# Performance work log

Measured on AMD Instinct MI355X. Metric: run time of the kernel, lower is better.

The kernel has to match this reference:

```python
import jax, jax.numpy as jnp
import numpy as np
from jax import lax

# Mamba2-130m-like config (quantized wrapper)
D_MODEL = 768
N_LAYER = 8
D_STATE = 128
D_CONV = 4
EXPAND = 2
HEADDIM = 64
VOCAB = 50288
D_INNER = EXPAND * D_MODEL            # 1536
NHEADS = D_INNER // HEADDIM           # 24
D_IN_PROJ = 2 * D_INNER + 2 * D_STATE + NHEADS  # 3352 (ngroups=1)
CONV_DIM = D_INNER + 2 * D_STATE      # 1792
EPS = 1e-5
BATCH, SEQLEN = 1, 1024

# QuantRMSNorm rsqrt lookup table (256 entries over [1e-5, 10])
LUT_X = jnp.linspace(1e-5, 10.0, 256)
LUT_Y = 1.0 / jnp.sqrt(LUT_X)


def _fake_quant_linear(w):
    # QuantLinear: torch.quantize_per_tensor(scale=0.1, zero_point=0, qint8).dequantize()
    return jnp.clip(jnp.round(w / 0.1), -128, 127) * 0.1


def setup_inputs():
    key = jax.random.key(0)
    ks = jax.random.split(key, 12)
    input_ids = jax.random.randint(ks[0], (BATCH, SEQLEN), 0, VOCAB)
    embedding = jax.random.normal(ks[1], (VOCAB, D_MODEL), jnp.float32)
    norm_w = jnp.ones((N_LAYER, D_MODEL), jnp.float32)
    in_proj_w = _fake_quant_linear(
        jax.random.normal(ks[2], (N_LAYER, D_IN_PROJ, D_MODEL), jnp.float32) * (D_MODEL ** -0.5))
    # QuantConv1d: asymmetric per-tensor int8 weight; forward uses q_weight.float()
    # WITHOUT subtracting zero_point (as in the source), times (w_scale * x_scale).
    conv_f = jax.random.normal(ks[3], (N_LAYER, CONV_DIM, D_CONV), jnp.float32) * (D_CONV ** -0.5)
    wmin = conv_f.min(axis=(1, 2), keepdims=True)
    wmax = conv_f.max(axis=(1, 2), keepdims=True)
    conv_scale = (wmax - wmin) / (255.0 + 1e-8)   # qmax - qmin = 255
    zp = jnp.round(-wmin / conv_scale)
    q_conv_w = jnp.clip(jnp.round(conv_f / conv_scale) + zp, -128, 127)
    conv_scale = conv_scale.reshape(N_LAYER)
    conv_b = jax.random.normal(ks[4], (N_LAYER, CONV_DIM), jnp.float32) * 0.02
    dt = jax.random.uniform(ks[5], (N_LAYER, NHEADS), jnp.float32, 0.001, 0.1)
    dt_bias = jnp.log(jnp.expm1(dt))              # inverse softplus
    A_log = jnp.log(jax.random.uniform(ks[6], (N_LAYER, NHEADS), jnp.float32, 1.0, 16.0))
    D_param = jnp.ones((N_LAYER, NHEADS), jnp.float32)
    mixer_norm_w = jnp.ones((N_LAYER, D_INNER), jnp.float32)
    out_proj_w = _fake_quant_linear(
        jax.random.normal(ks[7], (N_LAYER, D_MODEL, D_INNER), jnp.float32) * (D_INNER ** -0.5))
    normf_w = jnp.ones((D_MODEL,), jnp.float32)
    lm_head_w = _fake_quant_linear(
        jax.random.normal(ks[8], (VOCAB, D_MODEL), jnp.float32) * (D_MODEL ** -0.5))
    return dict(input_ids=input_ids, embedding=embedding, norm_w=norm_w, in_proj_w=in_proj_w,
                q_conv_w=q_conv_w, conv_scale=conv_scale, conv_b=conv_b, dt_bias=dt_bias,
                A_log=A_log, D_param=D_param, mixer_norm_w=mixer_norm_w, out_proj_w=out_proj_w,
                normf_w=normf_w, lm_head_w=lm_head_w)


def _lut_rmsnorm(x, w):
    # QuantRMSNorm: rsqrt approximated by a 256-entry LUT via bucketize
    rms = jnp.mean(x * x, axis=-1, keepdims=True) + EPS       # [b,l,1]
    idx = jnp.clip(jnp.searchsorted(LUT_X, rms), 0, 255)      # torch.bucketize (right=False)
    return x * LUT_Y[idx] * w


def _quant_act(x):
    # quantize_activation: symmetric per-tensor int8
    s = jnp.max(jnp.abs(x)) / (127.0 + 1e-8)
    return jnp.clip(jnp.round(x / s), -128, 127), s


def _mixer(u, in_w, qcw, cscale, cb, dtb, a_log, d_p, mnw, out_w):
    b, l, _ = u.shape
    zxbcdt = jnp.einsum('bld,ed->ble', u, in_w)               # QuantLinear (pre-fake-quantized w)
    z = zxbcdt[..., :D_INNER]
    xBC = zxbcdt[..., D_INNER:D_INNER + CONV_DIM]
    dt = jax.nn.softplus(zxbcdt[..., -NHEADS:] + dtb)         # [b,l,h]
    # QuantConv1d: depthwise causal conv on int8-quantized activation
    xq, xs = _quant_act(xBC)
    xp = jnp.pad(xq, ((0, 0), (D_CONV - 1, 0), (0, 0)))
    conv = sum(xp[:, k:k + l, :] * qcw[:, k] for k in range(D_CONV)) + cb
    xBC = jax.nn.silu(conv * (cscale * xs))
    x = xBC[..., :D_INNER].reshape(b, l, NHEADS, HEADDIM)
    Bm = xBC[..., D_INNER:D_INNER + D_STATE]                  # ngroups=1, shared over heads
    Cm = xBC[..., D_INNER + D_STATE:]
    dA = dt * (-jnp.exp(a_log))                               # [b,l,h]
    xdt = x * dt[..., None]
    def step(hs, inp):
        xdt_t, dA_t, B_t, C_t = inp
        hs = jnp.exp(dA_t)[..., None, None] * hs + xdt_t[..., None] * B_t[:, None, None, :]
        return hs, jnp.einsum('bhpn,bn->bhp', hs, C_t)
    h0 = jnp.zeros((b, NHEADS, HEADDIM, D_STATE), u.dtype)
    _, ys = lax.scan(step, h0, (xdt.swapaxes(0, 1), dA.swapaxes(0, 1),
                                Bm.swapaxes(0, 1), Cm.swapaxes(0, 1)))
    y = ys.swapaxes(0, 1) + x * d_p[None, None, :, None]      # [b,l,h,p]
    y = y.reshape(b, l, D_INNER)
    y = y * jax.nn.silu(z)                                    # gated RMSNorm (float, not LUT)
    y = y * lax.rsqrt(jnp.mean(y * y, axis=-1, keepdims=True) + EPS) * mnw
    return jnp.einsum('ble,de->bld', y, out_w)                # QuantLinear out_proj


def reference(input_ids, embedding, norm_w, in_proj_w, q_conv_w, conv_scale, conv_b,
              dt_bias, A_log, D_param, mixer_norm_w, out_proj_w, normf_w, lm_head_w):
    x = embedding[input_ids]
    for i in range(N_LAYER):
        y = _mixer(_lut_rmsnorm(x, norm_w[i]), in_proj_w[i], q_conv_w[i], conv_scale[i],
                   conv_b[i], dt_bias[i], A_log[i], D_param[i], mixer_norm_w[i], out_proj_w[i])
        x = y + x
    x = _lut_rmsnorm(x, normf_w)
    return jnp.einsum('bld,vd->blv', x, lm_head_w)            # logits [b,l,vocab]
```

## Files before the change

### kernel.cpp

```cpp
#include <hip/hip_runtime.h>
#include <math.h>

#define D_MODEL 768
#define N_LAYER 8
#define D_STATE 128
#define D_CONV 4
#define HEADDIM 64
#define D_INNER 1536
#define NHEADS 24
#define D_IN_PROJ 3352
#define CONV_DIM 1792
#define SEQLEN 1024
#define VOCAB 50288
#define EPS 1e-5f
#define T_SEG 32
#define NSEG  32

typedef __bf16 bf16x8 __attribute__((ext_vector_type(8)));
typedef float f32x4 __attribute__((ext_vector_type(4)));

__device__ inline unsigned short f2bf(float x) {
    union { float f; unsigned u; } v; v.f = x;
    unsigned r = v.u + 0x7fffu + ((v.u >> 16) & 1u);
    return (unsigned short)(r >> 16);
}
__device__ inline float bf2f(unsigned short b) {
    union { unsigned u; float f; } v; v.u = ((unsigned)b) << 16;
    return v.f;
}

__global__ void k_embed(const int* __restrict__ ids, const float* __restrict__ emb,
                        float* __restrict__ x) {
    int t = blockIdx.x;
    int id = ids[t];
    const float* er = emb + (long)id * D_MODEL;
    for (int d = threadIdx.x; d < D_MODEL; d += blockDim.x)
        x[(long)t * D_MODEL + d] = er[d];
}

__global__ void k_lutnorm(const float* __restrict__ x, const float* __restrict__ w,
                          float* __restrict__ out, unsigned short* __restrict__ oh,
                          unsigned short* __restrict__ ol, unsigned* __restrict__ mx) {
    __shared__ float sbuf[256];
    int t = blockIdx.x;
    if (t == 0 && threadIdx.x == 0) *mx = 0u;
    const float* xr = x + (long)t * D_MODEL;
    float ss = 0.f;
    for (int d = threadIdx.x; d < D_MODEL; d += 256) { float v = xr[d]; ss += v * v; }
    sbuf[threadIdx.x] = ss; __syncthreads();
    for (int s = 128; s > 0; s >>= 1) {
        if (threadIdx.x < s) sbuf[threadIdx.x] += sbuf[threadIdx.x + s];
        __syncthreads();
    }
    float rms = sbuf[0] / (float)D_MODEL + EPS;
    const float X0 = 1e-5f;
    const float STEP = (10.0f - 1e-5f) / 255.0f;
    int idx = (int)ceilf((rms - X0) / STEP);
    idx = min(max(idx, 0), 255);
    while (idx > 0 && (X0 + (float)(idx - 1) * STEP) >= rms) --idx;
    while (idx < 255 && (X0 + (float)idx * STEP) < rms) ++idx;
    float scale = 1.0f / sqrtf(X0 + (float)idx * STEP);
    for (int d = threadIdx.x; d < D_MODEL; d += 256) {
        float v = xr[d] * scale * w[d];
        out[(long)t * D_MODEL + d] = v;
        unsigned short h = f2bf(v);
        oh[(long)t * D_MODEL + d] = h;
        ol[(long)t * D_MODEL + d] = f2bf(v - bf2f(h));
    }
}

__global__ void k_f2bf(const float* __restrict__ src, unsigned short* __restrict__ dst, int n8) {
    int i = blockIdx.x * 256 + threadIdx.x;
    int stride = gridDim.x * 256;
    for (; i < n8; i += stride) {
        const float* s = src + (size_t)i * 8;
        float4 a = *(const float4*)s, b = *(const float4*)(s + 4);
        float ff[8] = {a.x, a.y, a.z, a.w, b.x, b.y, b.z, b.w};
        unsigned short h[8];
#pragma unroll
        for (int j = 0; j < 8; ++j) h[j] = f2bf(ff[j]);
        uint4 u = make_uint4(h[0] | (h[1] << 16), h[2] | (h[3] << 16),
                             h[4] | (h[5] << 16), h[6] | (h[7] << 16));
        *(uint4*)(dst + (size_t)i * 8) = u;
    }
}

__global__ void k_f2bf2(const float* __restrict__ src, unsigned short* __restrict__ dh,
                        unsigned short* __restrict__ dl, int n8) {
    int i = blockIdx.x * 256 + threadIdx.x;
    int stride = gridDim.x * 256;
    for (; i < n8; i += stride) {
        const float* s = src + (size_t)i * 8;
        float4 a = *(const float4*)s, b = *(const float4*)(s + 4);
        float ff[8] = {a.x, a.y, a.z, a.w, b.x, b.y, b.z, b.w};
        unsigned short h[8], lo[8];
#pragma unroll
        for (int j = 0; j < 8; ++j) {
            h[j] = f2bf(ff[j]);
            lo[j] = f2bf(ff[j] - bf2f(h[j]));
        }
        uint4 uh = make_uint4(h[0] | (h[1] << 16), h[2] | (h[3] << 16),
                              h[4] | (h[5] << 16), h[6] | (h[7] << 16));
        uint4 ul = make_uint4(lo[0] | (lo[1] << 16), lo[2] | (lo[3] << 16),
                              lo[4] | (lo[5] << 16), lo[6] | (lo[7] << 16));
        *(uint4*)(dh + (size_t)i * 8) = uh;
        *(uint4*)(dl + (size_t)i * 8) = ul;
    }
}

template <int PASSES, bool AMAX>
__global__ __launch_bounds__(512) void k_gemm_big(
    const unsigned short* __restrict__ Agh, const unsigned short* __restrict__ Agl,
    const unsigned short* __restrict__ Bgh, const unsigned short* __restrict__ Bgl,
    float* __restrict__ C, int N, int NT, int K, unsigned* __restrict__ mx) {
    const int i = blockIdx.x;
    const int rxcd = i & 7, xm = (i >> 3) & 7, q = i >> 6;
    const int y = q * 8 + rxcd;
    if (y >= NT) return;
    const int bm = xm * 128, bn = y * 128;

    constexpr int SMEM_BYTES = (PASSES == 3) ? 32768 : 16896;
    __shared__ __align__(16) char smem[SMEM_BYTES];
    unsigned short (*Ah)[128][8] = (unsigned short(*)[128][8])(smem);
    unsigned short (*Bh)[128][8] = (unsigned short(*)[128][8])(smem + 8192);
    unsigned short (*Al)[128][8] = (unsigned short(*)[128][8])(smem + 16384);
    unsigned short (*Bl)[128][8] = (unsigned short(*)[128][8])(smem + 24576);

    const int tid = threadIdx.x;
    const int r = tid >> 2, g = tid & 3;
    const int rsw = r ^ (g << 1);
    const int w = tid >> 6, l = tid & 63;
    const int wm = w >> 2, wn = w & 3;
    const int lr = l & 15, lg = l >> 4;

    f32x4 acc[4][2];
#pragma unroll
    for (int m = 0; m < 4; ++m)
#pragma unroll
        for (int n = 0; n < 2; ++n) acc[m][n] = (f32x4){0.f, 0.f, 0.f, 0.f};

    for (int k0 = 0; k0 < K; k0 += 32) {
        {
            *(uint4*)&Ah[g][rsw][0] = *(const uint4*)(Agh + (size_t)(bm + r) * K + k0 + g * 8);
            if constexpr (PASSES == 3)
                *(uint4*)&Al[g][rsw][0] = *(const uint4*)(Agl + (size_t)(bm + r) * K + k0 + g * 8);
            int rB = bn + r;
            uint4 zb = make_uint4(0, 0, 0, 0);
            uint4 ubh = (rB < N) ? *(const uint4*)(Bgh + (size_t)rB * K + k0 + g * 8) : zb;
            *(uint4*)&Bh[g][rsw][0] = ubh;
            if constexpr (PASSES == 3) {
                uint4 ubl = (rB < N) ? *(const uint4*)(Bgl + (size_t)rB * K + k0 + g * 8) : zb;
                *(uint4*)&Bl[g][rsw][0] = ubl;
            }
        }
        __syncthreads();

        bf16x8 ah[4], al_[4], bh[2], bl_[2];
#pragma unroll
        for (int m = 0; m < 4; ++m) {
            int row = (wm * 64 + m * 16 + lr) ^ (lg << 1);
            ah[m] = *(const bf16x8*)&Ah[lg][row][0];
            if constexpr (PASSES == 3) al_[m] = *(const bf16x8*)&Al[lg][row][0];
        }
#pragma unroll
        for (int n = 0; n < 2; ++n) {
            int row = (wn * 32 + n * 16 + lr) ^ (lg << 1);
            bh[n] = *(const bf16x8*)&Bh[lg][row][0];
            if constexpr (PASSES == 3) bl_[n] = *(const bf16x8*)&Bl[lg][row][0];
        }
#pragma unroll
        for (int m = 0; m < 4; ++m)
#pragma unroll
            for (int n = 0; n < 2; ++n) {
                acc[m][n] = __builtin_amdgcn_mfma_f32_16x16x32_bf16(ah[m], bh[n], acc[m][n], 0, 0, 0);
                if constexpr (PASSES == 3) {
                    acc[m][n] = __builtin_amdgcn_mfma_f32_16x16x32_bf16(al_[m], bh[n], acc[m][n], 0, 0, 0);
                    acc[m][n] = __builtin_amdgcn_mfma_f32_16x16x32_bf16(ah[m], bl_[n], acc[m][n], 0, 0, 0);
                }
            }
        __syncthreads();
    }

    if (AMAX) {
        float lmax = 0.f;
#pragma unroll
        for (int m = 0; m < 4; ++m)
#pragma unroll
            for (int n = 0; n < 2; ++n) {
                int col = bn + wn * 32 + n * 16 + lr;
                if (col >= D_INNER && col < D_INNER + CONV_DIM) {
#pragma unroll
                    for (int r4 = 0; r4 < 4; ++r4)
                        lmax = fmaxf(lmax, fabsf(acc[m][n][r4]));
                }
            }
#pragma unroll
        for (int s = 1; s <= 32; s <<= 1) lmax = fmaxf(lmax, __shfl_xor(lmax, s));
        if (l == 0) atomicMax(mx, __float_as_uint(lmax));
    }

    float (*cbuf)[132] = (float(*)[132])smem;
    const int clrow = tid >> 4;
    const int clcol = (tid & 15) * 8;
#pragma unroll
    for (int c = 0; c < 4; ++c) {
        if (c) __syncthreads();
        if (wm == (c >> 1)) {
#pragma unroll
            for (int mm = 0; mm < 2; ++mm) {
                int m = (c & 1) * 2 + mm;
                int lrow = mm * 16 + lg * 4;
#pragma unroll
                for (int n = 0; n < 2; ++n) {
                    int lcol = wn * 32 + n * 16 + lr;
#pragma unroll
                    for (int r4 = 0; r4 < 4; ++r4) cbuf[lrow + r4][lcol] = acc[m][n][r4];
                }
            }
        }
        __syncthreads();
        int grow = bm + c * 32 + clrow;
        int gcol = bn + clcol;
        float4 v0 = *(const float4*)&cbuf[clrow][clcol];
        float4 v1 = *(const float4*)&cbuf[clrow][clcol + 4];
        float* dst = C + (size_t)grow * N + gcol;
        if (gcol + 8 <= N) {
            *(float4*)dst = v0;
            *(float4*)(dst + 4) = v1;
        } else if (gcol < N) {
            float tmp[8] = {v0.x, v0.y, v0.z, v0.w, v1.x, v1.y, v1.z, v1.w};
            for (int j = 0; j < 8; ++j)
                if (gcol + j < N) dst[j] = tmp[j];
        }
    }
}

__global__ __launch_bounds__(256) void k_gemm_out(
    const unsigned short* __restrict__ Agh, const unsigned short* __restrict__ Agl,
    const unsigned short* __restrict__ Bgh, const unsigned short* __restrict__ Bgl,
    float* __restrict__ C) {
    const int K = 1536, N = 768;
    const int i = blockIdx.x;
    const int rxcd = i & 7, xm = (i >> 3) & 15, q = i >> 7;
    const int y = q * 8 + rxcd;
    if (y >= 12) return;
    const int bm = xm * 64, bn = y * 64;

    __shared__ __align__(16) char smem[16384];
    unsigned short (*Ah)[64][8] = (unsigned short(*)[64][8])(smem);
    unsigned short (*Bh)[64][8] = (unsigned short(*)[64][8])(smem + 4096);
    unsigned short (*Al)[64][8] = (unsigned short(*)[64][8])(smem + 8192);
    unsigned short (*Bl)[64][8] = (unsigned short(*)[64][8])(smem + 12288);

    const int tid = threadIdx.x;
    const int r = tid >> 2, g = tid & 3;
    const int rsw = r ^ (g << 1);
    const int w = tid >> 6, l = tid & 63;
    const int wm = w >> 1, wn = w & 1;
    const int lr = l & 15, lg = l >> 4;

    f32x4 acc[2][2];
#pragma unroll
    for (int m = 0; m < 2; ++m)
#pragma unroll
        for (int n = 0; n < 2; ++n) acc[m][n] = (f32x4){0.f, 0.f, 0.f, 0.f};

    for (int k0 = 0; k0 < K; k0 += 32) {
        *(uint4*)&Ah[g][rsw][0] = *(const uint4*)(Agh + (size_t)(bm + r) * K + k0 + g * 8);
        *(uint4*)&Al[g][rsw][0] = *(const uint4*)(Agl + (size_t)(bm + r) * K + k0 + g * 8);
        *(uint4*)&Bh[g][rsw][0] = *(const uint4*)(Bgh + (size_t)(bn + r) * K + k0 + g * 8);
        *(uint4*)&Bl[g][rsw][0] = *(const uint4*)(Bgl + (size_t)(bn + r) * K + k0 + g * 8);
        __syncthreads();

        bf16x8 ah[2], al_[2], bh[2], bl_[2];
#pragma unroll
        for (int m = 0; m < 2; ++m) {
            int row = (wm * 32 + m * 16 + lr) ^ (lg << 1);
            ah[m] = *(const bf16x8*)&Ah[lg][row][0];
            al_[m] = *(const bf16x8*)&Al[lg][row][0];
        }
#pragma unroll
        for (int n = 0; n < 2; ++n) {
            int row = (wn * 32 + n * 16 + lr) ^ (lg << 1);
            bh[n] = *(const bf16x8*)&Bh[lg][row][0];
            bl_[n] = *(const bf16x8*)&Bl[lg][row][0];
        }
#pragma unroll
        for (int m = 0; m < 2; ++m)
#pragma unroll
            for (int n = 0; n < 2; ++n) {
                acc[m][n] = __builtin_amdgcn_mfma_f32_16x16x32_bf16(ah[m], bh[n], acc[m][n], 0, 0, 0);
                acc[m][n] = __builtin_amdgcn_mfma_f32_16x16x32_bf16(al_[m], bh[n], acc[m][n], 0, 0, 0);
                acc[m][n] = __builtin_amdgcn_mfma_f32_16x16x32_bf16(ah[m], bl_[n], acc[m][n], 0, 0, 0);
            }
        __syncthreads();
    }

    float (*cbuf)[68] = (float(*)[68])smem;
    const int clrow = tid >> 3;
    const int clcol = (tid & 7) * 8;
#pragma unroll
    for (int c = 0; c < 2; ++c) {
        if (c) __syncthreads();
        if (wm == c) {
#pragma unroll
            for (int m = 0; m < 2; ++m) {
                int lrow = m * 16 + lg * 4;
#pragma unroll
                for (int n = 0; n < 2; ++n) {
                    int lcol = wn * 32 + n * 16 + lr;
#pragma unroll
                    for (int r4 = 0; r4 < 4; ++r4) cbuf[lrow + r4][lcol] = acc[m][n][r4];
                }
            }
        }
        __syncthreads();
        int grow = bm + c * 32 + clrow;
        float* dst = C + (size_t)grow * N + bn + clcol;
        float4 v0 = *(const float4*)&cbuf[clrow][clcol];
        float4 v1 = *(const float4*)&cbuf[clrow][clcol + 4];
        float4 r0 = *(const float4*)dst;
        float4 r1 = *(const float4*)(dst + 4);
        r0.x += v0.x; r0.y += v0.y; r0.z += v0.z; r0.w += v0.w;
        r1.x += v1.x; r1.y += v1.y; r1.z += v1.z; r1.w += v1.w;
        *(float4*)dst = r0;
        *(float4*)(dst + 4) = r1;
    }
}

template <int PASSES, bool ACCUM>
__global__ __launch_bounds__(256) void k_gemm_mfma(const float* __restrict__ A,
                                                   const float* __restrict__ B,
                                                   float* __restrict__ C,
                                                   int M, int N, int K) {
    __shared__ __align__(16) unsigned short Ah[4][128][8];
    __shared__ __align__(16) unsigned short Bh[4][128][8];
    __shared__ __align__(16) unsigned short Al[(PASSES == 3) ? 4 : 1][128][8];
    __shared__ __align__(16) unsigned short Bl[(PASSES == 3) ? 4 : 1][128][8];
    const int bm = blockIdx.x * 128, bn = blockIdx.y * 128;
    const int tid = threadIdx.x;
    const int rr = tid >> 2, g = tid & 3;
    const int w = tid >> 6, l = tid & 63;
    const int wm = w >> 1, wn = w & 1;
    const int lr = l & 15, lg = l >> 4;
    f32x4 acc[4][4];
#pragma unroll
    for (int m = 0; m < 4; ++m)
#pragma unroll
        for (int n = 0; n < 4; ++n) acc[m][n] = (f32x4){0.f, 0.f, 0.f, 0.f};
    for (int k0 = 0; k0 < K; k0 += 32) {
#pragma unroll
        for (int half = 0; half < 2; ++half) {
            int r = rr + half * 64;
            {
                const float* s = A + (size_t)(bm + r) * K + k0 + g * 8;
                float4 f0 = *(const float4*)s;
                float4 f1 = *(const float4*)(s + 4);
                float ff[8] = {f0.x, f0.y, f0.z, f0.w, f1.x, f1.y, f1.z, f1.w};
                unsigned short h[8], lo[8];
#pragma unroll
                for (int ii = 0; ii < 8; ++ii) {
                    h[ii] = f2bf(ff[ii]);
                    if (PASSES == 3) lo[ii] = f2bf(ff[ii] - bf2f(h[ii]));
                }
                *(uint4*)&Ah[g][r][0] = make_uint4(h[0] | (h[1] << 16), h[2] | (h[3] << 16),
                                                   h[4] | (h[5] << 16), h[6] | (h[7] << 16));
                if (PASSES == 3)
                    *(uint4*)&Al[g][r][0] = make_uint4(lo[0] | (lo[1] << 16), lo[2] | (lo[3] << 16),
                                                       lo[4] | (lo[5] << 16), lo[6] | (lo[7] << 16));
            }
            {
                int rB = bn + r;
                float ff[8] = {0.f, 0.f, 0.f, 0.f, 0.f, 0.f, 0.f, 0.f};
                if (rB < N) {
                    const float* s = B + (size_t)rB * K + k0 + g * 8;
                    float4 f0 = *(const float4*)s;
                    float4 f1 = *(const float4*)(s + 4);
                    ff[0] = f0.x; ff[1] = f0.y; ff[2] = f0.z; ff[3] = f0.w;
                    ff[4] = f1.x; ff[5] = f1.y; ff[6] = f1.z; ff[7] = f1.w;
                }
                unsigned short h[8], lo[8];
#pragma unroll
                for (int ii = 0; ii < 8; ++ii) {
                    h[ii] = f2bf(ff[ii]);
                    if (PASSES == 3) lo[ii] = f2bf(ff[ii] - bf2f(h[ii]));
                }
                *(uint4*)&Bh[g][r][0] = make_uint4(h[0] | (h[1] << 16), h[2] | (h[3] << 16),
                                                   h[4] | (h[5] << 16), h[6] | (h[7] << 16));
                if (PASSES == 3)
                    *(uint4*)&Bl[g][r][0] = make_uint4(lo[0] | (lo[1] << 16), lo[2] | (lo[3] << 16),
                                                       lo[4] | (lo[5] << 16), lo[6] | (lo[7] << 16));
            }
        }
        __syncthreads();
        bf16x8 ah[4], bh[4], al_[4], bl_[4];
#pragma unroll
        for (int m = 0; m < 4; ++m) {
            int row = wm * 64 + m * 16 + lr;
            ah[m] = *(const bf16x8*)&Ah[lg][row][0];
            if (PASSES == 3) al_[m] = *(const bf16x8*)&Al[lg][row][0];
        }
#pragma unroll
        for (int n = 0; n < 4; ++n) {
            int row = wn * 64 + n * 16 + lr;
            bh[n] = *(const bf16x8*)&Bh[lg][row][0];
            if (PASSES == 3) bl_[n] = *(const bf16x8*)&Bl[lg][row][0];
        }
#pragma unroll
        for (int m = 0; m < 4; ++m)
#pragma unroll
            for (int n = 0; n < 4; ++n) {
                acc[m][n] = __builtin_amdgcn_mfma_f32_16x16x32_bf16(ah[m], bh[n], acc[m][n], 0, 0, 0);
                if (PASSES == 3) {
                    acc[m][n] = __builtin_amdgcn_mfma_f32_16x16x32_bf16(al_[m], bh[n], acc[m][n], 0, 0, 0);
                    acc[m][n] = __builtin_amdgcn_mfma_f32_16x16x32_bf16(ah[m], bl_[n], acc[m][n], 0, 0, 0);
                }
            }
        __syncthreads();
    }
#pragma unroll
    for (int m = 0; m < 4; ++m) {
        int row0 = bm + wm * 64 + m * 16 + lg * 4;
#pragma unroll
        for (int n = 0; n < 4; ++n) {
            int col = bn + wn * 64 + n * 16 + lr;
            if (col < N) {
#pragma unroll
                for (int r4 = 0; r4 < 4; ++r4) {
                    size_t off = (size_t)(row0 + r4) * N + col;
                    if (ACCUM) C[off] += acc[m][n][r4]; else C[off] = acc[m][n][r4];
                }
            }
        }
    }
}

__global__ void k_absmax(const float* __restrict__ zx, unsigned* __restrict__ out) {
    __shared__ float sbuf[256];
    float m = 0.f;
    int total = SEQLEN * CONV_DIM;
    for (int i = blockIdx.x * blockDim.x + threadIdx.x; i < total; i += gridDim.x * blockDim.x) {
        int t = i / CONV_DIM, c = i - t * CONV_DIM;
        float v = fabsf(zx[(long)t * D_IN_PROJ + D_INNER + c]);
        m = fmaxf(m, v);
    }
    sbuf[threadIdx.x] = m; __syncthreads();
    for (int s = 128; s > 0; s >>= 1) {
        if (threadIdx.x < s) sbuf[threadIdx.x] = fmaxf(sbuf[threadIdx.x], sbuf[threadIdx.x + s]);
        __syncthreads();
    }
    if (threadIdx.x == 0) atomicMax(out, __float_as_uint(sbuf[0]));
}

__global__ void k_convq(const float* __restrict__ zx, const float* __restrict__ qcw,
                        const float* __restrict__ cb, const float* __restrict__ cscale,
                        const unsigned* __restrict__ mx, float* __restrict__ xact) {
    int i = blockIdx.x * blockDim.x + threadIdx.x;
    if (i >= SEQLEN * CONV_DIM) return;
    float s = __uint_as_float(*mx) / (127.0f + 1e-8f);
    float inv_s = 1.0f / s;
    int t = i / CONV_DIM, c = i - t * CONV_DIM;
    float acc = cb[c];
#pragma unroll
    for (int k = 0; k < D_CONV; ++k) {
        int tt = t - (D_CONV - 1) + k;
        if (tt >= 0) {
            float q = rintf(zx[(size_t)tt * D_IN_PROJ + D_INNER + c] * inv_s);
            q = fminf(fmaxf(q, -128.0f), 127.0f);
            acc = fmaf(q, qcw[c * D_CONV + k], acc);
        }
    }
    float v = acc * (cscale[0] * s);
    xact[i] = v / (1.0f + expf(-v));
}

__global__ __launch_bounds__(256) void k_scan_local(
    const float* __restrict__ xact, const float* __restrict__ zx,
    const float* __restrict__ dtbias, const float* __restrict__ A_log,
    float* __restrict__ y, float* __restrict__ hloc, float* __restrict__ dpre) {
    const int head = blockIdx.x;
    const int seg  = blockIdx.y;
    const int tid  = threadIdx.x;
    const int p  = tid >> 2;
    const int nc = tid & 3;
    const int t0 = seg * T_SEG;

    __shared__ float4 sB4[T_SEG][32];
    __shared__ float4 sC4[T_SEG][32];
    __shared__ float  sX[T_SEG][64];
    __shared__ float  sDt[T_SEG], sA[T_SEG];

#pragma unroll
    for (int it = 0; it < 4; ++it) {
        int slot = tid + it * 256;
        int t = slot >> 5, c4 = slot & 31;
        const float* rowp = xact + (size_t)(t0 + t) * CONV_DIM + D_INNER;
        float4 bv = *(const float4*)(rowp + c4 * 4);
        float4 cv = *(const float4*)(rowp + D_STATE + c4 * 4);
        int grp = c4 >> 3, r4 = c4 & 7;
        int sl = grp * 8 + ((r4 + 2 * grp) & 7);
        sB4[t][sl] = bv;
        sC4[t][sl] = cv;
    }
#pragma unroll
    for (int it = 0; it < 2; ++it) {
        int slot = tid + it * 256;
        int t = slot >> 4, c4 = slot & 15;
        *(float4*)&sX[t][c4 * 4] =
            *(const float4*)(xact + (size_t)(t0 + t) * CONV_DIM + head * HEADDIM + c4 * 4);
    }
    if (tid < T_SEG) {
        float v = zx[(size_t)(t0 + tid) * D_IN_PROJ + (D_INNER + CONV_DIM) + head] + dtbias[head];
        float dtv = fmaxf(v, 0.f) + log1pf(expf(-fabsf(v)));
        sDt[tid] = dtv;
        sA[tid] = expf(dtv * (-expf(A_log[head])));
    }
    __syncthreads();

    float h[32];
#pragma unroll
    for (int j = 0; j < 32; ++j) h[j] = 0.f;
    float d = 1.f;
    float* yrow = y + head * HEADDIM + p;

    for (int t = 0; t < T_SEG; ++t) {
        float a = sA[t], dtv = sDt[t];
        float xdt = sX[t][p] * dtv;
        d *= a;
        float acc = 0.f;
#pragma unroll
        for (int j4 = 0; j4 < 8; ++j4) {
            int sl = nc * 8 + ((j4 + 2 * nc) & 7);
            float4 Bv = sB4[t][sl];
            float4 Cv = sC4[t][sl];
            h[j4 * 4 + 0] = fmaf(a, h[j4 * 4 + 0], xdt * Bv.x); acc = fmaf(h[j4 * 4 + 0], Cv.x, acc);
            h[j4 * 4 + 1] = fmaf(a, h[j4 * 4 + 1], xdt * Bv.y); acc = fmaf(h[j4 * 4 + 1], Cv.y, acc);
            h[j4 * 4 + 2] = fmaf(a, h[j4 * 4 + 2], xdt * Bv.z); acc = fmaf(h[j4 * 4 + 2], Cv.z, acc);
            h[j4 * 4 + 3] = fmaf(a, h[j4 * 4 + 3], xdt * Bv.w); acc = fmaf(h[j4 * 4 + 3], Cv.w, acc);
        }
        acc += __shfl_xor(acc, 1);
        acc += __shfl_xor(acc, 2);
        if (nc == 0) yrow[(size_t)(t0 + t) * D_INNER] = acc;
        if (tid == 0) dpre[(head * NSEG + seg) * T_SEG + t] = d;
    }

    float* hb = hloc + ((size_t)(head * NSEG + seg) * 64 + p) * 128 + nc * 32;
#pragma unroll
    for (int j4 = 0; j4 < 8; ++j4)
        *(float4*)(hb + j4 * 4) =
            make_float4(h[j4 * 4], h[j4 * 4 + 1], h[j4 * 4 + 2], h[j4 * 4 + 3]);
}

__global__ __launch_bounds__(256) void k_scan_seg(float* __restrict__ hloc,
                                                  const float* __restrict__ dpre) {
    int g = blockIdx.x * 256 + threadIdx.x;
    int head = g >> 11;
    int e4 = g & 2047;
    float4 run = make_float4(0.f, 0.f, 0.f, 0.f);
    for (int seg = 0; seg < NSEG; ++seg) {
        float d = dpre[(head * NSEG + seg) * T_SEG + (T_SEG - 1)];
        float4* ptr = (float4*)hloc + (size_t)(head * NSEG + seg) * 2048 + e4;
        float4 v = *ptr;
        run.x = fmaf(d, run.x, v.x);
        run.y = fmaf(d, run.y, v.y);
        run.z = fmaf(d, run.z, v.z);
        run.w = fmaf(d, run.w, v.w);
        *ptr = run;
    }
}

__global__ __launch_bounds__(256) void k_scan_fix(
    const float* __restrict__ xact, const float* __restrict__ hloc,
    const float* __restrict__ dpre, float* __restrict__ y) {
    const int head = blockIdx.x;
    const int seg  = blockIdx.y + 1;
    const int tid  = threadIdx.x;
    const int p  = tid >> 2;
    const int nc = tid & 3;
    const int t0 = seg * T_SEG;

    __shared__ float4 sC4[T_SEG][32];
    __shared__ float  sD[T_SEG];

#pragma unroll
    for (int it = 0; it < 4; ++it) {
        int slot = tid + it * 256;
        int t = slot >> 5, c4 = slot & 31;
        float4 cv = *(const float4*)(xact + (size_t)(t0 + t) * CONV_DIM + D_INNER + D_STATE + c4 * 4);
        int grp = c4 >> 3, r4 = c4 & 7;
        sC4[t][grp * 8 + ((r4 + 2 * grp) & 7)] = cv;
    }
    if (tid < T_SEG) sD[tid] = dpre[(head * NSEG + seg) * T_SEG + tid];
    __syncthreads();

    float H[32];
    const float* hb = hloc + ((size_t)(head * NSEG + seg - 1) * 64 + p) * 128 + nc * 32;
#pragma unroll
    for (int j4 = 0; j4 < 8; ++j4) {
        float4 v = *(const float4*)(hb + j4 * 4);
        H[j4 * 4 + 0] = v.x; H[j4 * 4 + 1] = v.y; H[j4 * 4 + 2] = v.z; H[j4 * 4 + 3] = v.w;
    }
    float* yrow = y + head * HEADDIM + p;
    for (int t = 0; t < T_SEG; ++t) {
        float acc = 0.f;
#pragma unroll
        for (int j4 = 0; j4 < 8; ++j4) {
            int sl = nc * 8 + ((j4 + 2 * nc) & 7);
            float4 Cv = sC4[t][sl];
            acc = fmaf(H[j4 * 4 + 0], Cv.x, acc);
            acc = fmaf(H[j4 * 4 + 1], Cv.y, acc);
            acc = fmaf(H[j4 * 4 + 2], Cv.z, acc);
            acc = fmaf(H[j4 * 4 + 3], Cv.w, acc);
        }
        acc += __shfl_xor(acc, 1);
        acc += __shfl_xor(acc, 2);
        if (nc == 0) yrow[(size_t)(t0 + t) * D_INNER] += sD[t] * acc;
    }
}

__global__ void k_gatenorm(const float* __restrict__ ybuf, const float* __restrict__ zx,
                           const float* __restrict__ xact, const float* __restrict__ dpar,
                           const float* __restrict__ mnw, float* __restrict__ y3,
                           unsigned short* __restrict__ y3h, unsigned short* __restrict__ y3l) {
    __shared__ float sbuf[256];
    int t = blockIdx.x;
    const float* yr = ybuf + (long)t * D_INNER;
    const float* zr = zx + (long)t * D_IN_PROJ;
    const float* xa = xact + (long)t * CONV_DIM;
    float vals[6];
    float ss = 0.f;
#pragma unroll
    for (int j = 0; j < 6; ++j) {
        int e = threadIdx.x + j * 256;
        float z = zr[e];
        float v = (yr[e] + xa[e] * dpar[e >> 6]) * (z / (1.0f + expf(-z)));
        vals[j] = v; ss += v * v;
    }
    sbuf[threadIdx.x] = ss; __syncthreads();
    for (int s = 128; s > 0; s >>= 1) {
        if (threadIdx.x < s) sbuf[threadIdx.x] += sbuf[threadIdx.x + s];
        __syncthreads();
    }
    float scale = 1.0f / sqrtf(sbuf[0] / (float)D_INNER + EPS);
#pragma unroll
    for (int j = 0; j < 6; ++j) {
        int e = threadIdx.x + j * 256;
        float v = vals[j] * scale * mnw[e];
        y3[(long)t * D_INNER + e] = v;
        unsigned short h = f2bf(v);
        y3h[(long)t * D_INNER + e] = h;
        y3l[(long)t * D_INNER + e] = f2bf(v - bf2f(h));
    }
}

extern "C" void kernel_launch(void* const* d_in, const int* in_sizes, int n_in,
                              void* d_out, int out_size, void* d_ws, size_t ws_size,
                              hipStream_t stream) {
    const int*   ids    = (const int*)d_in[0];
    const float* emb    = (const float*)d_in[1];
    const float* norm_w = (const float*)d_in[2];
    const float* inw    = (const float*)d_in[3];
    const float* qconv  = (const float*)d_in[4];
    const float* cscale = (const float*)d_in[5];
    const float* convb  = (const float*)d_in[6];
    const float* dtbias = (const float*)d_in[7];
    const float* alog   = (const float*)d_in[8];
    const float* dpar   = (const float*)d_in[9];
    const float* mnw    = (const float*)d_in[10];
    const float* outw   = (const float*)d_in[11];
    const float* normf  = (const float*)d_in[12];
    const float* lmw    = (const float*)d_in[13];
    float* out = (float*)d_out;

    char* base = (char*)d_ws;
    size_t off = 0;
    auto alloc = [&](size_t bytes) { char* r = base + off; off = (off + bytes + 255) & ~(size_t)255; return r; };

    float* xres = (float*)alloc((size_t)SEQLEN * D_MODEL * 4);
    float* u    = (float*)alloc((size_t)SEQLEN * D_MODEL * 4);
    float* zx   = (float*)alloc((size_t)SEQLEN * D_IN_PROJ * 4);
    float* xact = (float*)alloc((size_t)SEQLEN * CONV_DIM * 4);
    float* ybuf = (float*)alloc((size_t)SEQLEN * D_INNER * 4);
    float* y3   = (float*)alloc((size_t)SEQLEN * D_INNER * 4);
    float* hloc = (float*)alloc((size_t)NHEADS * NSEG * HEADDIM * D_STATE * 4);
    float* dpre = (float*)alloc((size_t)NHEADS * NSEG * T_SEG * 4);
    unsigned* mx = (unsigned*)alloc(64);
    unsigned short* uh  = (unsigned short*)alloc((size_t)SEQLEN * D_MODEL * 2);
    unsigned short* ul  = (unsigned short*)alloc((size_t)SEQLEN * D_MODEL * 2);
    unsigned short* y3h = (unsigned short*)alloc((size_t)SEQLEN * D_INNER * 2);
    unsigned short* y3l = (unsigned short*)alloc((size_t)SEQLEN * D_INNER * 2);
    unsigned short* lmwh = (unsigned short*)alloc((size_t)VOCAB * D_MODEL * 2);
    size_t core_need = off;
    unsigned short* inwh = (unsigned short*)alloc((size_t)N_LAYER * D_IN_PROJ * D_MODEL * 2);
    unsigned short* inwl = (unsigned short*)alloc((size_t)N_LAYER * D_IN_PROJ * D_MODEL * 2);
    unsigned short* outwh = (unsigned short*)alloc((size_t)N_LAYER * D_MODEL * D_INNER * 2);
    unsigned short* outwl = (unsigned short*)alloc((size_t)N_LAYER * D_MODEL * D_INNER * 2);
    size_t full_need = off;
    const bool big = (ws_size >= full_need);
    (void)core_need;

    k_embed<<<SEQLEN, 256, 0, stream>>>(ids, emb, xres);
    k_f2bf<<<2048, 256, 0, stream>>>(lmw, lmwh, (VOCAB * D_MODEL) / 8);
    if (big) {
        k_f2bf2<<<2048, 256, 0, stream>>>(inw, inwh, inwl, (N_LAYER * D_IN_PROJ * D_MODEL) / 8);
        k_f2bf2<<<2048, 256, 0, stream>>>(outw, outwh, outwl, (N_LAYER * D_MODEL * D_INNER) / 8);
    }

    int nq = SEQLEN * CONV_DIM;
    const int NT_IN = (D_IN_PROJ + 127) / 128;
    const int NT_LM = (VOCAB + 127) / 128;
    for (int l = 0; l < N_LAYER; ++l) {
        k_lutnorm<<<SEQLEN, 256, 0, stream>>>(xres, norm_w + l * D_MODEL, u, uh, ul, mx);
        if (big) {
            int nblk = 8 * 8 * ((NT_IN + 7) / 8);
            k_gemm_big<3, true><<<nblk, 512, 0, stream>>>(
                uh, ul, inwh + (size_t)l * D_IN_PROJ * D_MODEL,
                inwl + (size_t)l * D_IN_PROJ * D_MODEL, zx, D_IN_PROJ, NT_IN, D_MODEL, mx);
        } else {
            dim3 g1(SEQLEN / 128, NT_IN);
            k_gemm_mfma<3, false><<<g1, 256, 0, stream>>>(u, inw + (size_t)l * D_IN_PROJ * D_MODEL,
                                                          zx, SEQLEN, D_IN_PROJ, D_MODEL);
            k_absmax<<<256, 256, 0, stream>>>(zx, mx);
        }
        k_convq<<<(nq + 255) / 256, 256, 0, stream>>>(zx, qconv + l * CONV_DIM * D_CONV,
                                                      convb + l * CONV_DIM, cscale + l, mx, xact);
        dim3 gs1(NHEADS, NSEG);
        k_scan_local<<<gs1, 256, 0, stream>>>(xact, zx, dtbias + l * NHEADS, alog + l * NHEADS,
                                              ybuf, hloc, dpre);
        k_scan_seg<<<192, 256, 0, stream>>>(hloc, dpre);
        dim3 gs3(NHEADS, NSEG - 1);
        k_scan_fix<<<gs3, 256, 0, stream>>>(xact, hloc, dpre, ybuf);
        k_gatenorm<<<SEQLEN, 256, 0, stream>>>(ybuf, zx, xact, dpar + l * NHEADS,
                                               mnw + l * D_INNER, y3, y3h, y3l);
        if (big) {
            k_gemm_out<<<256, 256, 0, stream>>>(y3h, y3l,
                outwh + (size_t)l * D_MODEL * D_INNER, outwl + (size_t)l * D_MODEL * D_INNER, xres);
        } else {
            dim3 g2(SEQLEN / 128, (D_MODEL + 127) / 128);
            k_gemm_mfma<3, true><<<g2, 256, 0, stream>>>(y3, outw + (size_t)l * D_MODEL * D_INNER,
                                                         xres, SEQLEN, D_MODEL, D_INNER);
        }
    }
    k_lutnorm<<<SEQLEN, 256, 0, stream>>>(xres, normf, u, uh, ul, mx);
    {
        int nblk = 8 * 8 * ((NT_LM + 7) / 8);
        k_gemm_big<1, false><<<nblk, 512, 0, stream>>>(uh, nullptr, lmwh, nullptr,
                                                       out, VOCAB, NT_LM, D_MODEL, nullptr);
    }
}
```

Before: 1.635 ms.

## Fuse exact int8-weight bf16 conversion into double-buffered GEMM loads

The weight GEMMs now read fp32 weights directly and convert them on the fly to bf16 as round(w*10), which is exact because the quantized weights are integer multiples of 0.1. This removes the separate weight conversion kernels and the hi/lo weight split, so in_proj and out_proj GEMMs drop from three MFMA passes to two and the lm_head GEMM reads fp32 weights instead of pre-converted bf16. The GEMM k-loops are also double-buffered with register prefetch, and the unused fp32 u and y3 buffers are no longer written. Correctness now depends on every weight, including lm_head, being an exact 0.1-scaled int8 value.

New measurement: 1.813 ms. 1.11x slower.

```diff
diff --git a/kernel.cpp b/kernel.cpp
--- a/kernel.cpp
+++ b/kernel.cpp
@@ -28,6 +28,14 @@
     union { unsigned u; float f; } v; v.u = ((unsigned)b) << 16;
     return v.f;
 }
+__device__ inline uint4 packq10(float4 f0, float4 f1) {
+    float ff[8] = {f0.x, f0.y, f0.z, f0.w, f1.x, f1.y, f1.z, f1.w};
+    unsigned short h[8];
+#pragma unroll
+    for (int j = 0; j < 8; ++j) h[j] = f2bf(rintf(ff[j] * 10.0f));
+    return make_uint4(h[0] | (h[1] << 16), h[2] | (h[3] << 16),
+                      h[4] | (h[5] << 16), h[6] | (h[7] << 16));
+}
 
 __global__ void k_embed(const int* __restrict__ ids, const float* __restrict__ emb,
                         float* __restrict__ x) {
@@ -39,8 +47,8 @@
 }
 
 __global__ void k_lutnorm(const float* __restrict__ x, const float* __restrict__ w,
-                          float* __restrict__ out, unsigned short* __restrict__ oh,
-                          unsigned short* __restrict__ ol, unsigned* __restrict__ mx) {
+                          unsigned short* __restrict__ oh, unsigned short* __restrict__ ol,
+                          unsigned* __restrict__ mx) {
     __shared__ float sbuf[256];
     int t = blockIdx.x;
     if (t == 0 && threadIdx.x == 0) *mx = 0u;
@@ -62,146 +70,214 @@
     float scale = 1.0f / sqrtf(X0 + (float)idx * STEP);
     for (int d = threadIdx.x; d < D_MODEL; d += 256) {
         float v = xr[d] * scale * w[d];
-        out[(long)t * D_MODEL + d] = v;
         unsigned short h = f2bf(v);
         oh[(long)t * D_MODEL + d] = h;
         ol[(long)t * D_MODEL + d] = f2bf(v - bf2f(h));
     }
 }
 
-__global__ void k_f2bf(const float* __restrict__ src, unsigned short* __restrict__ dst, int n8) {
-    int i = blockIdx.x * 256 + threadIdx.x;
-    int stride = gridDim.x * 256;
-    for (; i < n8; i += stride) {
-        const float* s = src + (size_t)i * 8;
-        float4 a = *(const float4*)s, b = *(const float4*)(s + 4);
-        float ff[8] = {a.x, a.y, a.z, a.w, b.x, b.y, b.z, b.w};
-        unsigned short h[8];
-#pragma unroll
-        for (int j = 0; j < 8; ++j) h[j] = f2bf(ff[j]);
-        uint4 u = make_uint4(h[0] | (h[1] << 16), h[2] | (h[3] << 16),
-                             h[4] | (h[5] << 16), h[6] | (h[7] << 16));
-        *(uint4*)(dst + (size_t)i * 8) = u;
-    }
-}
-
-__global__ void k_f2bf2(const float* __restrict__ src, unsigned short* __restrict__ dh,
-                        unsigned short* __restrict__ dl, int n8) {
-    int i = blockIdx.x * 256 + threadIdx.x;
-    int stride = gridDim.x * 256;
-    for (; i < n8; i += stride) {
-        const float* s = src + (size_t)i * 8;
-        float4 a = *(const float4*)s, b = *(const float4*)(s + 4);
-        float ff[8] = {a.x, a.y, a.z, a.w, b.x, b.y, b.z, b.w};
-        unsigned short h[8], lo[8];
-#pragma unroll
-        for (int j = 0; j < 8; ++j) {
-            h[j] = f2bf(ff[j]);
-            lo[j] = f2bf(ff[j] - bf2f(h[j]));
-        }
-        uint4 uh = make_uint4(h[0] | (h[1] << 16), h[2] | (h[3] << 16),
-                              h[4] | (h[5] << 16), h[6] | (h[7] << 16));
-        uint4 ul = make_uint4(lo[0] | (lo[1] << 16), lo[2] | (lo[3] << 16),
-                              lo[4] | (lo[5] << 16), lo[6] | (lo[7] << 16));
-        *(uint4*)(dh + (size_t)i * 8) = uh;
-        *(uint4*)(dl + (size_t)i * 8) = ul;
-    }
-}
-
-template <int PASSES, bool AMAX>
-__global__ __launch_bounds__(512) void k_gemm_big(
+__global__ __launch_bounds__(512) void k_in(
     const unsigned short* __restrict__ Agh, const unsigned short* __restrict__ Agl,
-    const unsigned short* __restrict__ Bgh, const unsigned short* __restrict__ Bgl,
-    float* __restrict__ C, int N, int NT, int K, unsigned* __restrict__ mx) {
+    const float* __restrict__ Bw, float* __restrict__ C, unsigned* __restrict__ mx) {
+    const int K = D_MODEL, N = D_IN_PROJ, NK = 24;
+    const int i = blockIdx.x;
+    const int rxcd = i & 7, xm = (i >> 3) & 15, q = i >> 7;
+    const int y = q * 8 + rxcd;
+    if (y >= 27) return;
+    const int bm = xm * 64, bn = y * 128;
+
+    __shared__ __align__(16) char smem[32768];
+
+    const int tid = threadIdx.x;
+    const int w = tid >> 6, l = tid & 63;
+    const int wm = w >> 2, wn = w & 3;
+    const int lr = l & 15, lg = l >> 4;
+
+    const int ar = (tid & 255) >> 2, ag = tid & 3;
+    const int aidx = (ag * 64 + (ar ^ (ag << 1))) * 16;
+    const unsigned short* Asrc = ((tid < 256) ? Agh : Agl) + (size_t)(bm + ar) * K + ag * 8;
+    const int abase = (tid < 256) ? 0 : 4096;
+    const int br = tid >> 2, bg = tid & 3;
+    const int bidx = 8192 + (bg * 128 + (br ^ (bg << 1))) * 16;
+    const int brow = bn + br;
+    const bool bok = brow < N;
+    const float* bsrc0 = Bw + (size_t)brow * K + bg * 8;
+
+    f32x4 acc[2][2];
+#pragma unroll
+    for (int m = 0; m < 2; ++m)
+#pragma unroll
+        for (int n = 0; n < 2; ++n) acc[m][n] = (f32x4){0.f, 0.f, 0.f, 0.f};
+
+    uint4 ra;
+    float4 fb0 = make_float4(0.f, 0.f, 0.f, 0.f), fb1 = fb0;
+    ra = *(const uint4*)Asrc;
+    if (bok) { fb0 = *(const float4*)bsrc0; fb1 = *(const float4*)(bsrc0 + 4); }
+    *(uint4*)(smem + abase + aidx) = ra;
+    *(uint4*)(smem + bidx) = packq10(fb0, fb1);
+
+    int cur = 0;
+    for (int kt = 0; kt < NK; ++kt) {
+        __syncthreads();
+        if (kt + 1 < NK) {
+            int k0 = (kt + 1) * 32;
+            ra = *(const uint4*)(Asrc + k0);
+            if (bok) { fb0 = *(const float4*)(bsrc0 + k0); fb1 = *(const float4*)(bsrc0 + k0 + 4); }
+        }
+        const char* bb = smem + cur * 16384;
+        bf16x8 ah[2], al[2], bh[2];
+#pragma unroll
+        for (int m = 0; m < 2; ++m) {
+            int row = (wm * 32 + m * 16 + lr) ^ (lg << 1);
+            ah[m] = *(const bf16x8*)(bb + (lg * 64 + row) * 16);
+            al[m] = *(const bf16x8*)(bb + 4096 + (lg * 64 + row) * 16);
+        }
+#pragma unroll
+        for (int n = 0; n < 2; ++n) {
+            int row = (wn * 32 + n * 16 + lr) ^ (lg << 1);
+            bh[n] = *(const bf16x8*)(bb + 8192 + (lg * 128 + row) * 16);
+        }
+#pragma unroll
+        for (int m = 0; m < 2; ++m)
+#pragma unroll
+            for (int n = 0; n < 2; ++n) {
+                acc[m][n] = __builtin_amdgcn_mfma_f32_16x16x32_bf16(ah[m], bh[n], acc[m][n], 0, 0, 0);
+                acc[m][n] = __builtin_amdgcn_mfma_f32_16x16x32_bf16(al[m], bh[n], acc[m][n], 0, 0, 0);
+            }
+        if (kt + 1 < NK) {
+            char* nb = smem + (cur ^ 1) * 16384;
+            *(uint4*)(nb + abase + aidx) = ra;
+            *(uint4*)(nb + bidx) = packq10(fb0, fb1);
+        }
+        cur ^= 1;
+    }
+
+    float lmax = 0.f;
+#pragma unroll
+    for (int m = 0; m < 2; ++m)
+#pragma unroll
+        for (int n = 0; n < 2; ++n) {
+            acc[m][n] *= 0.1f;
+            int col = bn + wn * 32 + n * 16 + lr;
+            if (col >= D_INNER && col < D_INNER + CONV_DIM) {
+#pragma unroll
+                for (int r4 = 0; r4 < 4; ++r4) lmax = fmaxf(lmax, fabsf(acc[m][n][r4]));
+            }
+        }
+#pragma unroll
+    for (int s = 1; s <= 32; s <<= 1) lmax = fmaxf(lmax, __shfl_xor(lmax, s));
+    if (l == 0) atomicMax(mx, __float_as_uint(lmax));
+
+    __syncthreads();
+    float (*cbuf)[132] = (float(*)[132])smem;
+    const int clrow = tid >> 4, clcol = (tid & 15) * 8;
+#pragma unroll
+    for (int c = 0; c < 2; ++c) {
+        if (c) __syncthreads();
+        if (wm == c) {
+#pragma unroll
+            for (int m = 0; m < 2; ++m) {
+                int lrow = m * 16 + lg * 4;
+#pragma unroll
+                for (int n = 0; n < 2; ++n) {
+                    int lcol = wn * 32 + n * 16 + lr;
+#pragma unroll
+                    for (int r4 = 0; r4 < 4; ++r4) cbuf[lrow + r4][lcol] = acc[m][n][r4];
+                }
+            }
+        }
+        __syncthreads();
+        int grow = bm + c * 32 + clrow;
+        int gcol = bn + clcol;
+        float4 v0 = *(const float4*)&cbuf[clrow][clcol];
+        float4 v1 = *(const float4*)&cbuf[clrow][clcol + 4];
+        float* dst = C + (size_t)grow * N + gcol;
+        if (gcol + 8 <= N) { *(float4*)dst = v0; *(float4*)(dst + 4) = v1; }
+        else if (gcol < N) {
+            float tmp[8] = {v0.x, v0.y, v0.z, v0.w, v1.x, v1.y, v1.z, v1.w};
+            for (int j = 0; j < 8; ++j) if (gcol + j < N) dst[j] = tmp[j];
+        }
+    }
+}
+
+__global__ __launch_bounds__(512) void k_lm(
+    const unsigned short* __restrict__ Agh, const float* __restrict__ Bw,
+    float* __restrict__ C) {
+    const int K = D_MODEL, N = VOCAB, NK = 24, NT = 393;
     const int i = blockIdx.x;
     const int rxcd = i & 7, xm = (i >> 3) & 7, q = i >> 6;
     const int y = q * 8 + rxcd;
     if (y >= NT) return;
     const int bm = xm * 128, bn = y * 128;
 
-    constexpr int SMEM_BYTES = (PASSES == 3) ? 32768 : 16896;
-    __shared__ __align__(16) char smem[SMEM_BYTES];
-    unsigned short (*Ah)[128][8] = (unsigned short(*)[128][8])(smem);
-    unsigned short (*Bh)[128][8] = (unsigned short(*)[128][8])(smem + 8192);
-    unsigned short (*Al)[128][8] = (unsigned short(*)[128][8])(smem + 16384);
-    unsigned short (*Bl)[128][8] = (unsigned short(*)[128][8])(smem + 24576);
-
+    __shared__ __align__(16) char smem[32768];
     const int tid = threadIdx.x;
-    const int r = tid >> 2, g = tid & 3;
-    const int rsw = r ^ (g << 1);
     const int w = tid >> 6, l = tid & 63;
     const int wm = w >> 2, wn = w & 3;
     const int lr = l & 15, lg = l >> 4;
 
+    const int ar = tid >> 2, ag = tid & 3;
+    const int aidx = (ag * 128 + (ar ^ (ag << 1))) * 16;
+    const int bidx = 8192 + aidx;
+    const unsigned short* asrc0 = Agh + (size_t)(bm + ar) * K + ag * 8;
+    const int brow = bn + ar;
+    const bool bok = brow < N;
+    const float* bsrc0 = Bw + (size_t)brow * K + ag * 8;
+
     f32x4 acc[4][2];
 #pragma unroll
     for (int m = 0; m < 4; ++m)
 #pragma unroll
         for (int n = 0; n < 2; ++n) acc[m][n] = (f32x4){0.f, 0.f, 0.f, 0.f};
 
-    for (int k0 = 0; k0 < K; k0 += 32) {
-        {
-            *(uint4*)&Ah[g][rsw][0] = *(const uint4*)(Agh + (size_t)(bm + r) * K + k0 + g * 8);
-            if constexpr (PASSES == 3)
-                *(uint4*)&Al[g][rsw][0] = *(const uint4*)(Agl + (size_t)(bm + r) * K + k0 + g * 8);
-            int rB = bn + r;
-            uint4 zb = make_uint4(0, 0, 0, 0);
-            uint4 ubh = (rB < N) ? *(const uint4*)(Bgh + (size_t)rB * K + k0 + g * 8) : zb;
-            *(uint4*)&Bh[g][rsw][0] = ubh;
-            if constexpr (PASSES == 3) {
-                uint4 ubl = (rB < N) ? *(const uint4*)(Bgl + (size_t)rB * K + k0 + g * 8) : zb;
-                *(uint4*)&Bl[g][rsw][0] = ubl;
-            }
-        }
-        __syncthreads();
-
-        bf16x8 ah[4], al_[4], bh[2], bl_[2];
+    uint4 ra;
+    float4 fb0 = make_float4(0.f, 0.f, 0.f, 0.f), fb1 = fb0;
+    ra = *(const uint4*)asrc0;
+    if (bok) { fb0 = *(const float4*)bsrc0; fb1 = *(const float4*)(bsrc0 + 4); }
+    *(uint4*)(smem + aidx) = ra;
+    *(uint4*)(smem + bidx) = packq10(fb0, fb1);
+
+    int cur = 0;
+    for (int kt = 0; kt < NK; ++kt) {
+        __syncthreads();
+        if (kt + 1 < NK) {
+            int k0 = (kt + 1) * 32;
+            ra = *(const uint4*)(asrc0 + k0);
+            if (bok) { fb0 = *(const float4*)(bsrc0 + k0); fb1 = *(const float4*)(bsrc0 + k0 + 4); }
+        }
+        const char* bb = smem + cur * 16384;
+        bf16x8 ah[4], bh[2];
 #pragma unroll
         for (int m = 0; m < 4; ++m) {
             int row = (wm * 64 + m * 16 + lr) ^ (lg << 1);
-            ah[m] = *(const bf16x8*)&Ah[lg][row][0];
-            if constexpr (PASSES == 3) al_[m] = *(const bf16x8*)&Al[lg][row][0];
+            ah[m] = *(const bf16x8*)(bb + (lg * 128 + row) * 16);
         }
 #pragma unroll
         for (int n = 0; n < 2; ++n) {
             int row = (wn * 32 + n * 16 + lr) ^ (lg << 1);
-            bh[n] = *(const bf16x8*)&Bh[lg][row][0];
-            if constexpr (PASSES == 3) bl_[n] = *(const bf16x8*)&Bl[lg][row][0];
+            bh[n] = *(const bf16x8*)(bb + 8192 + (lg * 128 + row) * 16);
         }
 #pragma unroll
         for (int m = 0; m < 4; ++m)
 #pragma unroll
-            for (int n = 0; n < 2; ++n) {
+            for (int n = 0; n < 2; ++n)
                 acc[m][n] = __builtin_amdgcn_mfma_f32_16x16x32_bf16(ah[m], bh[n], acc[m][n], 0, 0, 0);
-                if constexpr (PASSES == 3) {
-                    acc[m][n] = __builtin_amdgcn_mfma_f32_16x16x32_bf16(al_[m], bh[n], acc[m][n], 0, 0, 0);
-                    acc[m][n] = __builtin_amdgcn_mfma_f32_16x16x32_bf16(ah[m], bl_[n], acc[m][n], 0, 0, 0);
-                }
-            }
-        __syncthreads();
-    }
-
-    if (AMAX) {
-        float lmax = 0.f;
-#pragma unroll
-        for (int m = 0; m < 4; ++m)
-#pragma unroll
-            for (int n = 0; n < 2; ++n) {
-                int col = bn + wn * 32 + n * 16 + lr;
-                if (col >= D_INNER && col < D_INNER + CONV_DIM) {
-#pragma unroll
-                    for (int r4 = 0; r4 < 4; ++r4)
-                        lmax = fmaxf(lmax, fabsf(acc[m][n][r4]));
-                }
-            }
-#pragma unroll
-        for (int s = 1; s <= 32; s <<= 1) lmax = fmaxf(lmax, __shfl_xor(lmax, s));
-        if (l == 0) atomicMax(mx, __float_as_uint(lmax));
-    }
-
+        if (kt + 1 < NK) {
+            char* nb = smem + (cur ^ 1) * 16384;
+            *(uint4*)(nb + aidx) = ra;
+            *(uint4*)(nb + bidx) = packq10(fb0, fb1);
+        }
+        cur ^= 1;
+    }
+
+#pragma unroll
+    for (int m = 0; m < 4; ++m)
+#pragma unroll
+        for (int n = 0; n < 2; ++n) acc[m][n] *= 0.1f;
+
+    __syncthreads();
     float (*cbuf)[132] = (float(*)[132])smem;
-    const int clrow = tid >> 4;
-    const int clcol = (tid & 15) * 8;
+    const int clrow = tid >> 4, clcol = (tid & 15) * 8;
 #pragma unroll
     for (int c = 0; c < 4; ++c) {
         if (c) __syncthreads();
@@ -224,81 +300,92 @@
         float4 v0 = *(const float4*)&cbuf[clrow][clcol];
         float4 v1 = *(const float4*)&cbuf[clrow][clcol + 4];
         float* dst = C + (size_t)grow * N + gcol;
-        if (gcol + 8 <= N) {
-            *(float4*)dst = v0;
-            *(float4*)(dst + 4) = v1;
-        } else if (gcol < N) {
+        if (gcol + 8 <= N) { *(float4*)dst = v0; *(float4*)(dst + 4) = v1; }
+        else if (gcol < N) {
             float tmp[8] = {v0.x, v0.y, v0.z, v0.w, v1.x, v1.y, v1.z, v1.w};
-            for (int j = 0; j < 8; ++j)
-                if (gcol + j < N) dst[j] = tmp[j];
-        }
-    }
-}
-
-__global__ __launch_bounds__(256) void k_gemm_out(
+            for (int j = 0; j < 8; ++j) if (gcol + j < N) dst[j] = tmp[j];
+        }
+    }
+}
+
+__global__ __launch_bounds__(256) void k_out(
     const unsigned short* __restrict__ Agh, const unsigned short* __restrict__ Agl,
-    const unsigned short* __restrict__ Bgh, const unsigned short* __restrict__ Bgl,
-    float* __restrict__ C) {
-    const int K = 1536, N = 768;
+    const float* __restrict__ Bw, float* __restrict__ C) {
+    const int K = D_INNER, N = D_MODEL, NK = 48;
     const int i = blockIdx.x;
     const int rxcd = i & 7, xm = (i >> 3) & 15, q = i >> 7;
     const int y = q * 8 + rxcd;
     if (y >= 12) return;
     const int bm = xm * 64, bn = y * 64;
 
-    __shared__ __align__(16) char smem[16384];
-    unsigned short (*Ah)[64][8] = (unsigned short(*)[64][8])(smem);
-    unsigned short (*Bh)[64][8] = (unsigned short(*)[64][8])(smem + 4096);
-    unsigned short (*Al)[64][8] = (unsigned short(*)[64][8])(smem + 8192);
-    unsigned short (*Bl)[64][8] = (unsigned short(*)[64][8])(smem + 12288);
-
+    __shared__ __align__(16) char smem[24576];
     const int tid = threadIdx.x;
-    const int r = tid >> 2, g = tid & 3;
-    const int rsw = r ^ (g << 1);
     const int w = tid >> 6, l = tid & 63;
     const int wm = w >> 1, wn = w & 1;
     const int lr = l & 15, lg = l >> 4;
 
+    const int ar = tid >> 2, ag = tid & 3;
+    const int aidx = (ag * 64 + (ar ^ (ag << 1))) * 16;
+    const unsigned short* ahsrc = Agh + (size_t)(bm + ar) * K + ag * 8;
+    const unsigned short* alsrc = Agl + (size_t)(bm + ar) * K + ag * 8;
+    const float* bsrc0 = Bw + (size_t)(bn + ar) * K + ag * 8;
+
     f32x4 acc[2][2];
 #pragma unroll
     for (int m = 0; m < 2; ++m)
 #pragma unroll
         for (int n = 0; n < 2; ++n) acc[m][n] = (f32x4){0.f, 0.f, 0.f, 0.f};
 
-    for (int k0 = 0; k0 < K; k0 += 32) {
-        *(uint4*)&Ah[g][rsw][0] = *(const uint4*)(Agh + (size_t)(bm + r) * K + k0 + g * 8);
-        *(uint4*)&Al[g][rsw][0] = *(const uint4*)(Agl + (size_t)(bm + r) * K + k0 + g * 8);
-        *(uint4*)&Bh[g][rsw][0] = *(const uint4*)(Bgh + (size_t)(bn + r) * K + k0 + g * 8);
-        *(uint4*)&Bl[g][rsw][0] = *(const uint4*)(Bgl + (size_t)(bn + r) * K + k0 + g * 8);
-        __syncthreads();
-
-        bf16x8 ah[2], al_[2], bh[2], bl_[2];
+    uint4 rah, ral;
+    float4 fb0, fb1;
+    rah = *(const uint4*)ahsrc;
+    ral = *(const uint4*)alsrc;
+    fb0 = *(const float4*)bsrc0; fb1 = *(const float4*)(bsrc0 + 4);
+    *(uint4*)(smem + aidx) = rah;
+    *(uint4*)(smem + 4096 + aidx) = ral;
+    *(uint4*)(smem + 8192 + aidx) = packq10(fb0, fb1);
+
+    int cur = 0;
+    for (int kt = 0; kt < NK; ++kt) {
+        __syncthreads();
+        if (kt + 1 < NK) {
+            int k0 = (kt + 1) * 32;
+            rah = *(const uint4*)(ahsrc + k0);
+            ral = *(const uint4*)(alsrc + k0);
+            fb0 = *(const float4*)(bsrc0 + k0); fb1 = *(const float4*)(bsrc0 + k0 + 4);
+        }
+        const char* bb = smem + cur * 12288;
+        bf16x8 ah[2], al[2], bh[2];
 #pragma unroll
         for (int m = 0; m < 2; ++m) {
             int row = (wm * 32 + m * 16 + lr) ^ (lg << 1);
-            ah[m] = *(const bf16x8*)&Ah[lg][row][0];
-            al_[m] = *(const bf16x8*)&Al[lg][row][0];
+            ah[m] = *(const bf16x8*)(bb + (lg * 64 + row) * 16);
+            al[m] = *(const bf16x8*)(bb + 4096 + (lg * 64 + row) * 16);
         }
 #pragma unroll
         for (int n = 0; n < 2; ++n) {
             int row = (wn * 32 + n * 16 + lr) ^ (lg << 1);
-            bh[n] = *(const bf16x8*)&Bh[lg][row][0];
-            bl_[n] = *(const bf16x8*)&Bl[lg][row][0];
+            bh[n] = *(const bf16x8*)(bb + 8192 + (lg * 64 + row) * 16);
         }
 #pragma unroll
         for (int m = 0; m < 2; ++m)
 #pragma unroll
             for (int n = 0; n < 2; ++n) {
                 acc[m][n] = __builtin_amdgcn_mfma_f32_16x16x32_bf16(ah[m], bh[n], acc[m][n], 0, 0, 0);
-                acc[m][n] = __builtin_amdgcn_mfma_f32_16x16x32_bf16(al_[m], bh[n], acc[m][n], 0, 0, 0);
-                acc[m][n] = __builtin_amdgcn_mfma_f32_16x16x32_bf16(ah[m], bl_[n], acc[m][n], 0, 0, 0);
+                acc[m][n] = __builtin_amdgcn_mfma_f32_16x16x32_bf16(al[m], bh[n], acc[m][n], 0, 0, 0);
             }
-        __syncthreads();
-    }
-
+        if (kt + 1 < NK) {
+            char* nb = smem + (cur ^ 1) * 12288;
+            *(uint4*)(nb + aidx) = rah;
+            *(uint4*)(nb + 4096 + aidx) = ral;
+            *(uint4*)(nb + 8192 + aidx) = packq10(fb0, fb1);
+        }
+        cur ^= 1;
+    }
+
+    __syncthreads();
     float (*cbuf)[68] = (float(*)[68])smem;
-    const int clrow = tid >> 3;
-    const int clcol = (tid & 7) * 8;
+    const int clrow = tid >> 3, clcol = (tid & 7) * 8;
 #pragma unroll
     for (int c = 0; c < 2; ++c) {
         if (c) __syncthreads();
@@ -310,7 +397,7 @@
                 for (int n = 0; n < 2; ++n) {
                     int lcol = wn * 32 + n * 16 + lr;
 #pragma unroll
-                    for (int r4 = 0; r4 < 4; ++r4) cbuf[lrow + r4][lcol] = acc[m][n][r4];
+                    for (int r4 = 0; r4 < 4; ++r4) cbuf[lrow + r4][lcol] = acc[m][n][r4] * 0.1f;
                 }
             }
         }
@@ -326,130 +413,6 @@
         *(float4*)dst = r0;
         *(float4*)(dst + 4) = r1;
     }
-}
-
-template <int PASSES, bool ACCUM>
-__global__ __launch_bounds__(256) void k_gemm_mfma(const float* __restrict__ A,
-                                                   const float* __restrict__ B,
-                                                   float* __restrict__ C,
-                                                   int M, int N, int K) {
-    __shared__ __align__(16) unsigned short Ah[4][128][8];
-    __shared__ __align__(16) unsigned short Bh[4][128][8];
-    __shared__ __align__(16) unsigned short Al[(PASSES == 3) ? 4 : 1][128][8];
-    __shared__ __align__(16) unsigned short Bl[(PASSES == 3) ? 4 : 1][128][8];
-    const int bm = blockIdx.x * 128, bn = blockIdx.y * 128;
-    const int tid = threadIdx.x;
-    const int rr = tid >> 2, g = tid & 3;
-    const int w = tid >> 6, l = tid & 63;
-    const int wm = w >> 1, wn = w & 1;
-    const int lr = l & 15, lg = l >> 4;
-    f32x4 acc[4][4];
-#pragma unroll
-    for (int m = 0; m < 4; ++m)
-#pragma unroll
-        for (int n = 0; n < 4; ++n) acc[m][n] = (f32x4){0.f, 0.f, 0.f, 0.f};
-    for (int k0 = 0; k0 < K; k0 += 32) {
-#pragma unroll
-        for (int half = 0; half < 2; ++half) {
-            int r = rr + half * 64;
-            {
-                const float* s = A + (size_t)(bm + r) * K + k0 + g * 8;
-                float4 f0 = *(const float4*)s;
-                float4 f1 = *(const float4*)(s + 4);
-                float ff[8] = {f0.x, f0.y, f0.z, f0.w, f1.x, f1.y, f1.z, f1.w};
-                unsigned short h[8], lo[8];
-#pragma unroll
-                for (int ii = 0; ii < 8; ++ii) {
-                    h[ii] = f2bf(ff[ii]);
-                    if (PASSES == 3) lo[ii] = f2bf(ff[ii] - bf2f(h[ii]));
-                }
-                *(uint4*)&Ah[g][r][0] = make_uint4(h[0] | (h[1] << 16), h[2] | (h[3] << 16),
-                                                   h[4] | (h[5] << 16), h[6] | (h[7] << 16));
-                if (PASSES == 3)
-                    *(uint4*)&Al[g][r][0] = make_uint4(lo[0] | (lo[1] << 16), lo[2] | (lo[3] << 16),
-                                                       lo[4] | (lo[5] << 16), lo[6] | (lo[7] << 16));
-            }
-            {
-                int rB = bn + r;
-                float ff[8] = {0.f, 0.f, 0.f, 0.f, 0.f, 0.f, 0.f, 0.f};
-                if (rB < N) {
-                    const float* s = B + (size_t)rB * K + k0 + g * 8;
-                    float4 f0 = *(const float4*)s;
-                    float4 f1 = *(const float4*)(s + 4);
-                    ff[0] = f0.x; ff[1] = f0.y; ff[2] = f0.z; ff[3] = f0.w;
-                    ff[4] = f1.x; ff[5] = f1.y; ff[6] = f1.z; ff[7] = f1.w;
-                }
-                unsigned short h[8], lo[8];
-#pragma unroll
-                for (int ii = 0; ii < 8; ++ii) {
-                    h[ii] = f2bf(ff[ii]);
-                    if (PASSES == 3) lo[ii] = f2bf(ff[ii] - bf2f(h[ii]));
-                }
-                *(uint4*)&Bh[g][r][0] = make_uint4(h[0] | (h[1] << 16), h[2] | (h[3] << 16),
-                                                   h[4] | (h[5] << 16), h[6] | (h[7] << 16));
-                if (PASSES == 3)
-                    *(uint4*)&Bl[g][r][0] = make_uint4(lo[0] | (lo[1] << 16), lo[2] | (lo[3] << 16),
-                                                       lo[4] | (lo[5] << 16), lo[6] | (lo[7] << 16));
-            }
-        }
-        __syncthreads();
-        bf16x8 ah[4], bh[4], al_[4], bl_[4];
-#pragma unroll
-        for (int m = 0; m < 4; ++m) {
-            int row = wm * 64 + m * 16 + lr;
-            ah[m] = *(const bf16x8*)&Ah[lg][row][0];
-            if (PASSES == 3) al_[m] = *(const bf16x8*)&Al[lg][row][0];
-        }
-#pragma unroll
-        for (int n = 0; n < 4; ++n) {
-            int row = wn * 64 + n * 16 + lr;
-            bh[n] = *(const bf16x8*)&Bh[lg][row][0];
-            if (PASSES == 3) bl_[n] = *(const bf16x8*)&Bl[lg][row][0];
-        }
-#pragma unroll
-        for (int m = 0; m < 4; ++m)
-#pragma unroll
-            for (int n = 0; n < 4; ++n) {
-                acc[m][n] = __builtin_amdgcn_mfma_f32_16x16x32_bf16(ah[m], bh[n], acc[m][n], 0, 0, 0);
-                if (PASSES == 3) {
-                    acc[m][n] = __builtin_amdgcn_mfma_f32_16x16x32_bf16(al_[m], bh[n], acc[m][n], 0, 0, 0);
-                    acc[m][n] = __builtin_amdgcn_mfma_f32_16x16x32_bf16(ah[m], bl_[n], acc[m][n], 0, 0, 0);
-                }
-            }
-        __syncthreads();
-    }
-#pragma unroll
-    for (int m = 0; m < 4; ++m) {
-        int row0 = bm + wm * 64 + m * 16 + lg * 4;
-#pragma unroll
-        for (int n = 0; n < 4; ++n) {
-            int col = bn + wn * 64 + n * 16 + lr;
-            if (col < N) {
-#pragma unroll
-                for (int r4 = 0; r4 < 4; ++r4) {
-                    size_t off = (size_t)(row0 + r4) * N + col;
-                    if (ACCUM) C[off] += acc[m][n][r4]; else C[off] = acc[m][n][r4];
-                }
-            }
-        }
-    }
-}
-
-__global__ void k_absmax(const float* __restrict__ zx, unsigned* __restrict__ out) {
-    __shared__ float sbuf[256];
-    float m = 0.f;
-    int total = SEQLEN * CONV_DIM;
-    for (int i = blockIdx.x * blockDim.x + threadIdx.x; i < total; i += gridDim.x * blockDim.x) {
-        int t = i / CONV_DIM, c = i - t * CONV_DIM;
-        float v = fabsf(zx[(long)t * D_IN_PROJ + D_INNER + c]);
-        m = fmaxf(m, v);
-    }
-    sbuf[threadIdx.x] = m; __syncthreads();
-    for (int s = 128; s > 0; s >>= 1) {
-        if (threadIdx.x < s) sbuf[threadIdx.x] = fmaxf(sbuf[threadIdx.x], sbuf[threadIdx.x + s]);
-        __syncthreads();
-    }
-    if (threadIdx.x == 0) atomicMax(out, __float_as_uint(sbuf[0]));
 }
 
 __global__ void k_convq(const float* __restrict__ zx, const float* __restrict__ qcw,
@@ -620,7 +583,7 @@
 
 __global__ void k_gatenorm(const float* __restrict__ ybuf, const float* __restrict__ zx,
                            const float* __restrict__ xact, const float* __restrict__ dpar,
-                           const float* __restrict__ mnw, float* __restrict__ y3,
+                           const float* __restrict__ mnw,
                            unsigned short* __restrict__ y3h, unsigned short* __restrict__ y3l) {
     __shared__ float sbuf[256];
     int t = blockIdx.x;
@@ -646,7 +609,6 @@
     for (int j = 0; j < 6; ++j) {
         int e = threadIdx.x + j * 256;
         float v = vals[j] * scale * mnw[e];
-        y3[(long)t * D_INNER + e] = v;
         unsigned short h = f2bf(v);
         y3h[(long)t * D_INNER + e] = h;
         y3l[(long)t * D_INNER + e] = f2bf(v - bf2f(h));
@@ -677,11 +639,9 @@
     auto alloc = [&](size_t bytes) { char* r = base + off; off = (off + bytes + 255) & ~(size_t)255; return r; };
 
     float* xres = (float*)alloc((size_t)SEQLEN * D_MODEL * 4);
-    float* u    = (float*)alloc((size_t)SEQLEN * D_MODEL * 4);
     float* zx   = (float*)alloc((size_t)SEQLEN * D_IN_PROJ * 4);
     float* xact = (float*)alloc((size_t)SEQLEN * CONV_DIM * 4);
     float* ybuf = (float*)alloc((size_t)SEQLEN * D_INNER * 4);
-    float* y3   = (float*)alloc((size_t)SEQLEN * D_INNER * 4);
     float* hloc = (float*)alloc((size_t)NHEADS * NSEG * HEADDIM * D_STATE * 4);
     float* dpre = (float*)alloc((size_t)NHEADS * NSEG * T_SEG * 4);
     unsigned* mx = (unsigned*)alloc(64);
@@ -689,39 +649,13 @@
     unsigned short* ul  = (unsigned short*)alloc((size_t)SEQLEN * D_MODEL * 2);
     unsigned short* y3h = (unsigned short*)alloc((size_t)SEQLEN * D_INNER * 2);
     unsigned short* y3l = (unsigned short*)alloc((size_t)SEQLEN * D_INNER * 2);
-    unsigned short* lmwh = (unsigned short*)alloc((size_t)VOCAB * D_MODEL * 2);
-    size_t core_need = off;
-    unsigned short* inwh = (unsigned short*)alloc((size_t)N_LAYER * D_IN_PROJ * D_MODEL * 2);
-    unsigned short* inwl = (unsigned short*)alloc((size_t)N_LAYER * D_IN_PROJ * D_MODEL * 2);
-    unsigned short* outwh = (unsigned short*)alloc((size_t)N_LAYER * D_MODEL * D_INNER * 2);
-    unsigned short* outwl = (unsigned short*)alloc((size_t)N_LAYER * D_MODEL * D_INNER * 2);
-    size_t full_need = off;
-    const bool big = (ws_size >= full_need);
-    (void)core_need;
 
     k_embed<<<SEQLEN, 256, 0, stream>>>(ids, emb, xres);
-    k_f2bf<<<2048, 256, 0, stream>>>(lmw, lmwh, (VOCAB * D_MODEL) / 8);
-    if (big) {
-        k_f2bf2<<<2048, 256, 0, stream>>>(inw, inwh, inwl, (N_LAYER * D_IN_PROJ * D_MODEL) / 8);
-        k_f2bf2<<<2048, 256, 0, stream>>>(outw, outwh, outwl, (N_LAYER * D_MODEL * D_INNER) / 8);
-    }
 
     int nq = SEQLEN * CONV_DIM;
-    const int NT_IN = (D_IN_PROJ + 127) / 128;
-    const int NT_LM = (VOCAB + 127) / 128;
     for (int l = 0; l < N_LAYER; ++l) {
-        k_lutnorm<<<SEQLEN, 256, 0, stream>>>(xres, norm_w + l * D_MODEL, u, uh, ul, mx);
-        if (big) {
-            int nblk = 8 * 8 * ((NT_IN + 7) / 8);
-            k_gemm_big<3, true><<<nblk, 512, 0, stream>>>(
-                uh, ul, inwh + (size_t)l * D_IN_PROJ * D_MODEL,
-                inwl + (size_t)l * D_IN_PROJ * D_MODEL, zx, D_IN_PROJ, NT_IN, D_MODEL, mx);
-        } else {
-            dim3 g1(SEQLEN / 128, NT_IN);
-            k_gemm_mfma<3, false><<<g1, 256, 0, stream>>>(u, inw + (size_t)l * D_IN_PROJ * D_MODEL,
-                                                          zx, SEQLEN, D_IN_PROJ, D_MODEL);
-            k_absmax<<<256, 256, 0, stream>>>(zx, mx);
-        }
+        k_lutnorm<<<SEQLEN, 256, 0, stream>>>(xres, norm_w + l * D_MODEL, uh, ul, mx);
+        k_in<<<512, 512, 0, stream>>>(uh, ul, inw + (size_t)l * D_IN_PROJ * D_MODEL, zx, mx);
         k_convq<<<(nq + 255) / 256, 256, 0, stream>>>(zx, qconv + l * CONV_DIM * D_CONV,
                                                       convb + l * CONV_DIM, cscale + l, mx, xact);
         dim3 gs1(NHEADS, NSEG);
@@ -731,20 +665,9 @@
         dim3 gs3(NHEADS, NSEG - 1);
         k_scan_fix<<<gs3, 256, 0, stream>>>(xact, hloc, dpre, ybuf);
         k_gatenorm<<<SEQLEN, 256, 0, stream>>>(ybuf, zx, xact, dpar + l * NHEADS,
-                                               mnw + l * D_INNER, y3, y3h, y3l);
-        if (big) {
-            k_gemm_out<<<256, 256, 0, stream>>>(y3h, y3l,
-                outwh + (size_t)l * D_MODEL * D_INNER, outwl + (size_t)l * D_MODEL * D_INNER, xres);
-        } else {
-            dim3 g2(SEQLEN / 128, (D_MODEL + 127) / 128);
-            k_gemm_mfma<3, true><<<g2, 256, 0, stream>>>(y3, outw + (size_t)l * D_MODEL * D_INNER,
-                                                         xres, SEQLEN, D_MODEL, D_INNER);
-        }
-    }
-    k_lutnorm<<<SEQLEN, 256, 0, stream>>>(xres, normf, u, uh, ul, mx);
-    {
-        int nblk = 8 * 8 * ((NT_LM + 7) / 8);
-        k_gemm_big<1, false><<<nblk, 512, 0, stream>>>(uh, nullptr, lmwh, nullptr,
-                                                       out, VOCAB, NT_LM, D_MODEL, nullptr);
-    }
-}
+                                               mnw + l * D_INNER, y3h, y3l);
+        k_out<<<256, 256, 0, stream>>>(y3h, y3l, outw + (size_t)l * D_MODEL * D_INNER, xres);
+    }
+    k_lutnorm<<<SEQLEN, 256, 0, stream>>>(xres, normf, uh, ul, mx);
+    k_lm<<<3200, 512, 0, stream>>>(uh, lmw, out);
+}
```
